# Kernel tuning notes

Measured on AMD Instinct MI355X. Metric: run time of the kernel, lower is better.

## Reference

```python
import jax, jax.numpy as jnp
import numpy as np

B, N, D = 64, 5000, 128
EPS = 1e-5

def setup_inputs() -> dict:
    key = jax.random.key(0)
    ks = jax.random.split(key, 10)
    s = 1.0 / np.sqrt(D)
    s2 = 1.0 / np.sqrt(2 * D)
    return {
        "batch_size": B,
        "num_customers": N,
        "solution_neighbours": jax.random.randint(ks[0], (B, N, 2), 0, N + 1),
        "embeddings": jax.random.normal(ks[1], (B, N + 1, D), dtype=jnp.float32),
        "w_left": jax.random.uniform(ks[2], (D, D), jnp.float32, -s, s),
        "w_right": jax.random.uniform(ks[3], (D, D), jnp.float32, -s, s),
        "w_comb": jax.random.uniform(ks[4], (D, 2 * D), jnp.float32, -s2, s2),
        "b_comb": jax.random.uniform(ks[5], (D,), jnp.float32, -s2, s2),
        "w_ff": jax.random.uniform(ks[6], (D, D), jnp.float32, -s, s),
        "b_ff": jax.random.uniform(ks[7], (D,), jnp.float32, -s, s),
        "norm_w": jnp.ones((D,), jnp.float32),
        "norm_b": jnp.zeros((D,), jnp.float32),
    }

def _gather(emb, idx):
    # emb: (B, N+1, D), idx: (B, N) -> (B, N, D)
    d = emb.shape[-1]
    return jnp.take_along_axis(emb, jnp.broadcast_to(idx[:, :, None], idx.shape + (d,)), axis=1)

def reference(batch_size, num_customers, solution_neighbours, embeddings,
              w_left, w_right, w_comb, b_comb, w_ff, b_ff, norm_w, norm_b):
    left = _gather(embeddings, solution_neighbours[:, :, 0])
    right = _gather(embeddings, solution_neighbours[:, :, 1])
    # per-edge linear projections (directed graph: separate weights)
    info = left @ w_left.T + right @ w_right.T        # (B, N, D)
    cust = embeddings[:, 1:]                           # (B, N, D)
    combined = jnp.concatenate([cust, info], axis=2)   # (B, N, 2D)
    h = jax.nn.relu(combined @ w_comb.T + b_comb)
    h = h @ w_ff.T + b_ff
    # residual + InstanceNorm1d over the customer axis (per batch, per channel)
    added = cust + h
    mean = jnp.mean(added, axis=1, keepdims=True)
    var = jnp.mean(jnp.square(added - mean), axis=1, keepdims=True)  # biased var
    normed = (added - mean) * jax.lax.rsqrt(var + EPS) * norm_w + norm_b
    return jnp.concatenate([embeddings[:, :1], normed], axis=1)
```

## Files before the change

### kernel.cpp

```cpp
#include <hip/hip_runtime.h>

typedef unsigned short u16;
typedef __attribute__((ext_vector_type(8))) short bf16x8;
typedef __attribute__((ext_vector_type(4))) float f32x4;

#define BB 64
#define NN 5000
#define DD 128
#define EROW 640128
#define CROW 640000

__device__ __forceinline__ u16 f2bf(float f){
  unsigned u = __builtin_bit_cast(unsigned, f);
  u += 0x7fffu + ((u >> 16) & 1u);
  return (u16)(u >> 16);
}
__device__ __forceinline__ float bf2f(u16 h){
  unsigned u = ((unsigned)h) << 16;
  return __builtin_bit_cast(float, u);
}

__global__ __launch_bounds__(256) void k0_prep(
    const float* __restrict__ wl, const float* __restrict__ wr,
    const float* __restrict__ wcmb, const float* __restrict__ wff,
    const float* __restrict__ emb, float* __restrict__ out,
    u16* __restrict__ wbf, float* __restrict__ sums, float* __restrict__ sumsq)
{
  int t = blockIdx.x * 256 + threadIdx.x;
  if      (t < 16384) wbf[t] = f2bf(wl[t]);
  else if (t < 32768) wbf[t] = f2bf(wr[t - 16384]);
  else if (t < 65536) wbf[t] = f2bf(wcmb[t - 32768]);
  else                wbf[t] = f2bf(wff[t - 65536]);
  if (t < 8192){
    sums[t] = 0.f; sumsq[t] = 0.f;
    int b = t >> 7, d = t & 127;
    out[(size_t)b * EROW + d] = emb[(size_t)b * EROW + d];
  }
}

template<bool BF>
__global__ __launch_bounds__(256, 4)
void k1_main(const int2* __restrict__ sol, const float* __restrict__ emb,
             const u16* __restrict__ wbf, const float* __restrict__ b_comb,
             const float* __restrict__ b_ff, float* __restrict__ out,
             u16* __restrict__ abuf, float* __restrict__ sums, float* __restrict__ sumsq)
{
  const int tid  = threadIdx.x;
  const int lane = tid & 63;
  const int wave = tid >> 6;
  const int q    = lane >> 4;
  const int c    = lane & 15;
  const int tile = blockIdx.x;
  const int b    = blockIdx.y;
  const int rbase = tile * 64;
  const int RC = min(64, NN - rbase);

  __shared__ u16 A[64][136];
  __shared__ u16 Bb[64][136];
  __shared__ int sIL[64], sIR[64];

  if (tid < 64){
    int r = rbase + tid; r = min(r, NN - 1);
    int2 p = sol[(size_t)b * NN + r];
    sIL[tid] = p.x; sIR[tid] = p.y;
  }
  __syncthreads();

  const float* embB = emb + (size_t)b * EROW;
  const int gi = tid >> 2, gsub = tid & 3;

  {
    int il = sIL[gi], ir = sIR[gi];
    const float4* vL = (const float4*)(embB + (size_t)il * DD) + gsub * 8;
    const float4* vR = (const float4*)(embB + (size_t)ir * DD) + gsub * 8;
    #pragma unroll
    for (int j = 0; j < 8; ++j){
      float4 a = vL[j], bb = vR[j];
      int col = gsub * 32 + j * 4;
      ushort4 ua = {f2bf(a.x),  f2bf(a.y),  f2bf(a.z),  f2bf(a.w)};
      ushort4 ub = {f2bf(bb.x), f2bf(bb.y), f2bf(bb.z), f2bf(bb.w)};
      *(ushort4*)&A[gi][col]  = ua;
      *(ushort4*)&Bb[gi][col] = ub;
    }
  }
  __syncthreads();

  const int n0 = wave * 32 + c;
  const int n1 = n0 + 16;

  const u16* wl = wbf;
  const u16* wr = wbf + 16384;
  const u16* wc = wbf + 32768;
  const u16* wf = wbf + 65536;

  const f32x4 fz = {0.f, 0.f, 0.f, 0.f};
  f32x4 acc[4][2];

  #pragma unroll
  for (int mt = 0; mt < 4; ++mt){ acc[mt][0] = fz; acc[mt][1] = fz; }
  #pragma unroll
  for (int ks = 0; ks < 8; ++ks){
    const u16* W = (ks < 4) ? wl : wr;
    const int kk = (ks & 3) * 32 + q * 8;
    bf16x8 b0 = *(const bf16x8*)(W + n0 * 128 + kk);
    bf16x8 b1 = *(const bf16x8*)(W + n1 * 128 + kk);
    #pragma unroll
    for (int mt = 0; mt < 4; ++mt){
      bf16x8 a = *(const bf16x8*)&((ks < 4) ? A : Bb)[mt * 16 + c][kk];
      acc[mt][0] = __builtin_amdgcn_mfma_f32_16x16x32_bf16(a, b0, acc[mt][0], 0, 0, 0);
      acc[mt][1] = __builtin_amdgcn_mfma_f32_16x16x32_bf16(a, b1, acc[mt][1], 0, 0, 0);
    }
  }
  __syncthreads();

  #pragma unroll
  for (int mt = 0; mt < 4; ++mt){
    #pragma unroll
    for (int r = 0; r < 4; ++r){
      int m = mt * 16 + q * 4 + r;
      A[m][n0] = f2bf(acc[mt][0][r]);
      A[m][n1] = f2bf(acc[mt][1][r]);
    }
  }
  {
    int crow = min(rbase + gi + 1, NN);
    const float4* vC = (const float4*)(embB + (size_t)crow * DD) + gsub * 8;
    #pragma unroll
    for (int j = 0; j < 8; ++j){
      float4 cc = vC[j];
      int col = gsub * 32 + j * 4;
      ushort4 uc = {f2bf(cc.x), f2bf(cc.y), f2bf(cc.z), f2bf(cc.w)};
      *(ushort4*)&Bb[gi][col] = uc;
    }
  }
  __syncthreads();

  #pragma unroll
  for (int mt = 0; mt < 4; ++mt){ acc[mt][0] = fz; acc[mt][1] = fz; }
  #pragma unroll
  for (int ks = 0; ks < 8; ++ks){
    const int kk = (ks & 3) * 32 + q * 8;
    const int kg = ks * 32 + q * 8;
    bf16x8 b0 = *(const bf16x8*)(wc + n0 * 256 + kg);
    bf16x8 b1 = *(const bf16x8*)(wc + n1 * 256 + kg);
    #pragma unroll
    for (int mt = 0; mt < 4; ++mt){
      bf16x8 a = *(const bf16x8*)&((ks < 4) ? Bb : A)[mt * 16 + c][kk];
      acc[mt][0] = __builtin_amdgcn_mfma_f32_16x16x32_bf16(a, b0, acc[mt][0], 0, 0, 0);
      acc[mt][1] = __builtin_amdgcn_mfma_f32_16x16x32_bf16(a, b1, acc[mt][1], 0, 0, 0);
    }
  }
  __syncthreads();
  {
    float bc0 = b_comb[n0], bc1 = b_comb[n1];
    #pragma unroll
    for (int mt = 0; mt < 4; ++mt){
      #pragma unroll
      for (int r = 0; r < 4; ++r){
        int m = mt * 16 + q * 4 + r;
        A[m][n0] = f2bf(fmaxf(acc[mt][0][r] + bc0, 0.f));
        A[m][n1] = f2bf(fmaxf(acc[mt][1][r] + bc1, 0.f));
      }
    }
  }
  __syncthreads();

  #pragma unroll
  for (int mt = 0; mt < 4; ++mt){ acc[mt][0] = fz; acc[mt][1] = fz; }
  #pragma unroll
  for (int ks = 0; ks < 4; ++ks){
    const int kk = ks * 32 + q * 8;
    bf16x8 b0 = *(const bf16x8*)(wf + n0 * 128 + kk);
    bf16x8 b1 = *(const bf16x8*)(wf + n1 * 128 + kk);
    #pragma unroll
    for (int mt = 0; mt < 4; ++mt){
      bf16x8 a = *(const bf16x8*)&A[mt * 16 + c][kk];
      acc[mt][0] = __builtin_amdgcn_mfma_f32_16x16x32_bf16(a, b0, acc[mt][0], 0, 0, 0);
      acc[mt][1] = __builtin_amdgcn_mfma_f32_16x16x32_bf16(a, b1, acc[mt][1], 0, 0, 0);
    }
  }

  const float bf0 = b_ff[n0], bf1 = b_ff[n1];
  float sv0 = 0.f, sq0 = 0.f, sv1 = 0.f, sq1 = 0.f;
  float* outB = out + (size_t)b * EROW;
  #pragma unroll
  for (int mt = 0; mt < 4; ++mt){
    #pragma unroll
    for (int r = 0; r < 4; ++r){
      int m = mt * 16 + q * 4 + r;
      float v0 = acc[mt][0][r] + bf0 + bf2f(Bb[m][n0]);
      float v1 = acc[mt][1][r] + bf1 + bf2f(Bb[m][n1]);
      acc[mt][0][r] = v0; acc[mt][1][r] = v1;
      if (m < RC){
        sv0 += v0; sq0 += v0 * v0;
        sv1 += v1; sq1 += v1 * v1;
        if (!BF){
          size_t ro = (size_t)(rbase + m + 1) * DD;
          outB[ro + n0] = v0;
          outB[ro + n1] = v1;
        }
      }
    }
  }
  sv0 += __shfl_xor(sv0, 16); sv0 += __shfl_xor(sv0, 32);
  sq0 += __shfl_xor(sq0, 16); sq0 += __shfl_xor(sq0, 32);
  sv1 += __shfl_xor(sv1, 16); sv1 += __shfl_xor(sv1, 32);
  sq1 += __shfl_xor(sq1, 16); sq1 += __shfl_xor(sq1, 32);
  if (q == 0){
    atomicAdd(&sums [b * DD + n0], sv0);
    atomicAdd(&sumsq[b * DD + n0], sq0);
    atomicAdd(&sums [b * DD + n1], sv1);
    atomicAdd(&sumsq[b * DD + n1], sq1);
  }

  if (BF){
    __syncthreads();
    #pragma unroll
    for (int mt = 0; mt < 4; ++mt){
      #pragma unroll
      for (int r = 0; r < 4; ++r){
        int m = mt * 16 + q * 4 + r;
        A[m][n0] = f2bf(acc[mt][0][r]);
        A[m][n1] = f2bf(acc[mt][1][r]);
      }
    }
    __syncthreads();
    const int row = tid >> 2, cb = tid & 3;
    if (rbase + row < NN){
      u16* dst = abuf + ((size_t)b * NN + rbase + row) * DD + cb * 32;
      #pragma unroll
      for (int j = 0; j < 4; ++j)
        *(bf16x8*)(dst + j * 8) = *(const bf16x8*)&A[row][cb * 32 + j * 8];
    }
  }
}

__global__ __launch_bounds__(256) void k1b_stats(
    const float* __restrict__ sums, const float* __restrict__ sumsq,
    const float* __restrict__ nw, const float* __restrict__ nb,
    float* __restrict__ scale, float* __restrict__ shift)
{
  int t = blockIdx.x * 256 + threadIdx.x;
  int d = t & 127;
  float mean = sums[t] * (1.f / NN);
  float var  = sumsq[t] * (1.f / NN) - mean * mean;
  float inv  = rsqrtf(var + 1e-5f);
  float sc = inv * nw[d];
  scale[t] = sc;
  shift[t] = nb[d] - mean * sc;
}

__global__ __launch_bounds__(256) void k2_bf(
    const u16* __restrict__ abuf, const float* __restrict__ scale,
    const float* __restrict__ shift, float* __restrict__ out)
{
  const int b = blockIdx.y;
  const int e = (blockIdx.x * 256 + threadIdx.x) * 8;
  if (e >= CROW) return;
  const int d = e & 127;
  const uint4 raw = *(const uint4*)(abuf + (size_t)b * CROW + e);
  const float4 s0 = *(const float4*)&scale[b * DD + d];
  const float4 s1 = *(const float4*)&scale[b * DD + d + 4];
  const float4 h0 = *(const float4*)&shift[b * DD + d];
  const float4 h1 = *(const float4*)&shift[b * DD + d + 4];
  float4 v0, v1;
  v0.x = __builtin_bit_cast(float, raw.x << 16);
  v0.y = __builtin_bit_cast(float, raw.x & 0xffff0000u);
  v0.z = __builtin_bit_cast(float, raw.y << 16);
  v0.w = __builtin_bit_cast(float, raw.y & 0xffff0000u);
  v1.x = __builtin_bit_cast(float, raw.z << 16);
  v1.y = __builtin_bit_cast(float, raw.z & 0xffff0000u);
  v1.z = __builtin_bit_cast(float, raw.w << 16);
  v1.w = __builtin_bit_cast(float, raw.w & 0xffff0000u);
  v0.x = v0.x * s0.x + h0.x; v0.y = v0.y * s0.y + h0.y;
  v0.z = v0.z * s0.z + h0.z; v0.w = v0.w * s0.w + h0.w;
  v1.x = v1.x * s1.x + h1.x; v1.y = v1.y * s1.y + h1.y;
  v1.z = v1.z * s1.z + h1.z; v1.w = v1.w * s1.w + h1.w;
  float4* p = (float4*)(out + (size_t)b * EROW + DD + e);
  p[0] = v0; p[1] = v1;
}

__global__ __launch_bounds__(256) void k2_rmw(
    float* __restrict__ out, const float* __restrict__ scale, const float* __restrict__ shift)
{
  const int b = blockIdx.y;
  const int e = (blockIdx.x * 256 + threadIdx.x) * 8;
  if (e >= CROW) return;
  const int d = e & 127;
  const float4 s0 = *(const float4*)&scale[b * DD + d];
  const float4 s1 = *(const float4*)&scale[b * DD + d + 4];
  const float4 h0 = *(const float4*)&shift[b * DD + d];
  const float4 h1 = *(const float4*)&shift[b * DD + d + 4];
  float4* p = (float4*)(out + (size_t)b * EROW + DD + e);
  float4 v0 = p[0], v1 = p[1];
  v0.x = v0.x * s0.x + h0.x; v0.y = v0.y * s0.y + h0.y;
  v0.z = v0.z * s0.z + h0.z; v0.w = v0.w * s0.w + h0.w;
  v1.x = v1.x * s1.x + h1.x; v1.y = v1.y * s1.y + h1.y;
  v1.z = v1.z * s1.z + h1.z; v1.w = v1.w * s1.w + h1.w;
  p[0] = v0; p[1] = v1;
}

extern "C" void kernel_launch(void* const* d_in, const int* in_sizes, int n_in,
                              void* d_out, int out_size, void* d_ws, size_t ws_size,
                              hipStream_t stream)
{
  const int2*  sol  = (const int2*) d_in[2];
  const float* emb  = (const float*)d_in[3];
  const float* wl   = (const float*)d_in[4];
  const float* wr   = (const float*)d_in[5];
  const float* wcmb = (const float*)d_in[6];
  const float* bcmb = (const float*)d_in[7];
  const float* wff  = (const float*)d_in[8];
  const float* bff  = (const float*)d_in[9];
  const float* nw   = (const float*)d_in[10];
  const float* nb   = (const float*)d_in[11];
  float* out = (float*)d_out;

  u16*   wbf   = (u16*)d_ws;
  float* sums  = (float*)((char*)d_ws + 163840);
  float* sumsq = (float*)((char*)d_ws + 196608);
  float* scale = (float*)((char*)d_ws + 229376);
  float* shift = (float*)((char*)d_ws + 262144);
  u16*   abuf  = (u16*)((char*)d_ws + 294912);

  const size_t need = 294912ull + (size_t)BB * NN * DD * 2;
  const bool bfpath = (ws_size >= need);

  k0_prep <<<320, 256, 0, stream>>>(wl, wr, wcmb, wff, emb, out, wbf, sums, sumsq);
  if (bfpath){
    k1_main<true> <<<dim3(79, 64), 256, 0, stream>>>(sol, emb, wbf, bcmb, bff, out, abuf, sums, sumsq);
    k1b_stats<<<32, 256, 0, stream>>>(sums, sumsq, nw, nb, scale, shift);
    k2_bf  <<<dim3(313, 64), 256, 0, stream>>>(abuf, scale, shift, out);
  } else {
    k1_main<false><<<dim3(79, 64), 256, 0, stream>>>(sol, emb, wbf, bcmb, bff, out, abuf, sums, sumsq);
    k1b_stats<<<32, 256, 0, stream>>>(sums, sumsq, nw, nb, scale, shift);
    k2_rmw <<<dim3(313, 64), 256, 0, stream>>>(out, scale, shift);
  }
}
```

Measured before the change: 482.2 us.

## Prefetch gathers and weights into registers ahead of each MFMA stage

Issues all three embedding row loads (left, right, customer) up front and packs them to bf16 in registers. Weight fragments for the next GEMM stage are loaded into register arrays before the current stage's barrier, so global-load latency overlaps compute and LDS writes. Launch bounds occupancy drops from 4 to 3 blocks per SM to make room for the extra registers. The risk is lower occupancy and register pressure hiding less latency overall.

```diff
diff --git a/kernel.cpp b/kernel.cpp
--- a/kernel.cpp
+++ b/kernel.cpp
@@ -18,6 +18,14 @@
 __device__ __forceinline__ float bf2f(u16 h){
   unsigned u = ((unsigned)h) << 16;
   return __builtin_bit_cast(float, u);
+}
+__device__ __forceinline__ bf16x8 pack8(float4 a, float4 b){
+  bf16x8 r;
+  r[0] = (short)f2bf(a.x); r[1] = (short)f2bf(a.y);
+  r[2] = (short)f2bf(a.z); r[3] = (short)f2bf(a.w);
+  r[4] = (short)f2bf(b.x); r[5] = (short)f2bf(b.y);
+  r[6] = (short)f2bf(b.z); r[7] = (short)f2bf(b.w);
+  return r;
 }
 
 __global__ __launch_bounds__(256) void k0_prep(
@@ -39,7 +47,7 @@
 }
 
 template<bool BF>
-__global__ __launch_bounds__(256, 4)
+__global__ __launch_bounds__(256, 3)
 void k1_main(const int2* __restrict__ sol, const float* __restrict__ emb,
              const u16* __restrict__ wbf, const float* __restrict__ b_comb,
              const float* __restrict__ b_ff, float* __restrict__ out,
@@ -69,47 +77,69 @@
   const float* embB = emb + (size_t)b * EROW;
   const int gi = tid >> 2, gsub = tid & 3;
 
+  const int n0 = wave * 32 + c;
+  const int n1 = n0 + 16;
+
+  const u16* wl = wbf;
+  const u16* wr = wbf + 16384;
+  const u16* wc = wbf + 32768;
+  const u16* wf = wbf + 65536;
+
+  const float bc0 = b_comb[n0], bc1 = b_comb[n1];
+  const float bf0 = b_ff[n0],  bf1 = b_ff[n1];
+
+  float4 la[8], ra[8], ca[8];
   {
     int il = sIL[gi], ir = sIR[gi];
     const float4* vL = (const float4*)(embB + (size_t)il * DD) + gsub * 8;
     const float4* vR = (const float4*)(embB + (size_t)ir * DD) + gsub * 8;
-    #pragma unroll
-    for (int j = 0; j < 8; ++j){
-      float4 a = vL[j], bb = vR[j];
-      int col = gsub * 32 + j * 4;
-      ushort4 ua = {f2bf(a.x),  f2bf(a.y),  f2bf(a.z),  f2bf(a.w)};
-      ushort4 ub = {f2bf(bb.x), f2bf(bb.y), f2bf(bb.z), f2bf(bb.w)};
-      *(ushort4*)&A[gi][col]  = ua;
-      *(ushort4*)&Bb[gi][col] = ub;
-    }
-  }
-  __syncthreads();
-
-  const int n0 = wave * 32 + c;
-  const int n1 = n0 + 16;
-
-  const u16* wl = wbf;
-  const u16* wr = wbf + 16384;
-  const u16* wc = wbf + 32768;
-  const u16* wf = wbf + 65536;
+    int crow = min(rbase + gi + 1, NN);
+    const float4* vC = (const float4*)(embB + (size_t)crow * DD) + gsub * 8;
+    #pragma unroll
+    for (int j = 0; j < 8; ++j) la[j] = vL[j];
+    #pragma unroll
+    for (int j = 0; j < 8; ++j) ra[j] = vR[j];
+    #pragma unroll
+    for (int j = 0; j < 8; ++j) ca[j] = vC[j];
+  }
+  #pragma unroll
+  for (int j = 0; j < 4; ++j){
+    *(bf16x8*)&A [gi][gsub * 32 + j * 8] = pack8(la[2*j], la[2*j+1]);
+    *(bf16x8*)&Bb[gi][gsub * 32 + j * 8] = pack8(ra[2*j], ra[2*j+1]);
+  }
+  bf16x8 cw[4];
+  #pragma unroll
+  for (int j = 0; j < 4; ++j) cw[j] = pack8(ca[2*j], ca[2*j+1]);
+  __syncthreads();
 
   const f32x4 fz = {0.f, 0.f, 0.f, 0.f};
   f32x4 acc[4][2];
-
-  #pragma unroll
-  for (int mt = 0; mt < 4; ++mt){ acc[mt][0] = fz; acc[mt][1] = fz; }
+  bf16x8 w0[8], w1[8];
+
   #pragma unroll
   for (int ks = 0; ks < 8; ++ks){
     const u16* W = (ks < 4) ? wl : wr;
     const int kk = (ks & 3) * 32 + q * 8;
-    bf16x8 b0 = *(const bf16x8*)(W + n0 * 128 + kk);
-    bf16x8 b1 = *(const bf16x8*)(W + n1 * 128 + kk);
+    w0[ks] = *(const bf16x8*)(W + n0 * 128 + kk);
+    w1[ks] = *(const bf16x8*)(W + n1 * 128 + kk);
+  }
+  #pragma unroll
+  for (int mt = 0; mt < 4; ++mt){ acc[mt][0] = fz; acc[mt][1] = fz; }
+  #pragma unroll
+  for (int ks = 0; ks < 8; ++ks){
+    const int kk = (ks & 3) * 32 + q * 8;
     #pragma unroll
     for (int mt = 0; mt < 4; ++mt){
       bf16x8 a = *(const bf16x8*)&((ks < 4) ? A : Bb)[mt * 16 + c][kk];
-      acc[mt][0] = __builtin_amdgcn_mfma_f32_16x16x32_bf16(a, b0, acc[mt][0], 0, 0, 0);
-      acc[mt][1] = __builtin_amdgcn_mfma_f32_16x16x32_bf16(a, b1, acc[mt][1], 0, 0, 0);
-    }
+      acc[mt][0] = __builtin_amdgcn_mfma_f32_16x16x32_bf16(a, w0[ks], acc[mt][0], 0, 0, 0);
+      acc[mt][1] = __builtin_amdgcn_mfma_f32_16x16x32_bf16(a, w1[ks], acc[mt][1], 0, 0, 0);
+    }
+  }
+  #pragma unroll
+  for (int ks = 0; ks < 8; ++ks){
+    const int kg = ks * 32 + q * 8;
+    w0[ks] = *(const bf16x8*)(wc + n0 * 256 + kg);
+    w1[ks] = *(const bf16x8*)(wc + n1 * 256 + kg);
   }
   __syncthreads();
 
@@ -122,17 +152,9 @@
       A[m][n1] = f2bf(acc[mt][1][r]);
     }
   }
-  {
-    int crow = min(rbase + gi + 1, NN);
-    const float4* vC = (const float4*)(embB + (size_t)crow * DD) + gsub * 8;
-    #pragma unroll
-    for (int j = 0; j < 8; ++j){
-      float4 cc = vC[j];
-      int col = gsub * 32 + j * 4;
-      ushort4 uc = {f2bf(cc.x), f2bf(cc.y), f2bf(cc.z), f2bf(cc.w)};
-      *(ushort4*)&Bb[gi][col] = uc;
-    }
-  }
+  #pragma unroll
+  for (int j = 0; j < 4; ++j)
+    *(bf16x8*)&Bb[gi][gsub * 32 + j * 8] = cw[j];
   __syncthreads();
 
   #pragma unroll
@@ -140,47 +162,44 @@
   #pragma unroll
   for (int ks = 0; ks < 8; ++ks){
     const int kk = (ks & 3) * 32 + q * 8;
-    const int kg = ks * 32 + q * 8;
-    bf16x8 b0 = *(const bf16x8*)(wc + n0 * 256 + kg);
-    bf16x8 b1 = *(const bf16x8*)(wc + n1 * 256 + kg);
     #pragma unroll
     for (int mt = 0; mt < 4; ++mt){
       bf16x8 a = *(const bf16x8*)&((ks < 4) ? Bb : A)[mt * 16 + c][kk];
-      acc[mt][0] = __builtin_amdgcn_mfma_f32_16x16x32_bf16(a, b0, acc[mt][0], 0, 0, 0);
-      acc[mt][1] = __builtin_amdgcn_mfma_f32_16x16x32_bf16(a, b1, acc[mt][1], 0, 0, 0);
-    }
-  }
-  __syncthreads();
-  {
-    float bc0 = b_comb[n0], bc1 = b_comb[n1];
-    #pragma unroll
-    for (int mt = 0; mt < 4; ++mt){
-      #pragma unroll
-      for (int r = 0; r < 4; ++r){
-        int m = mt * 16 + q * 4 + r;
-        A[m][n0] = f2bf(fmaxf(acc[mt][0][r] + bc0, 0.f));
-        A[m][n1] = f2bf(fmaxf(acc[mt][1][r] + bc1, 0.f));
-      }
-    }
-  }
-  __syncthreads();
-
-  #pragma unroll
-  for (int mt = 0; mt < 4; ++mt){ acc[mt][0] = fz; acc[mt][1] = fz; }
+      acc[mt][0] = __builtin_amdgcn_mfma_f32_16x16x32_bf16(a, w0[ks], acc[mt][0], 0, 0, 0);
+      acc[mt][1] = __builtin_amdgcn_mfma_f32_16x16x32_bf16(a, w1[ks], acc[mt][1], 0, 0, 0);
+    }
+  }
   #pragma unroll
   for (int ks = 0; ks < 4; ++ks){
     const int kk = ks * 32 + q * 8;
-    bf16x8 b0 = *(const bf16x8*)(wf + n0 * 128 + kk);
-    bf16x8 b1 = *(const bf16x8*)(wf + n1 * 128 + kk);
+    w0[ks] = *(const bf16x8*)(wf + n0 * 128 + kk);
+    w1[ks] = *(const bf16x8*)(wf + n1 * 128 + kk);
+  }
+  __syncthreads();
+  #pragma unroll
+  for (int mt = 0; mt < 4; ++mt){
+    #pragma unroll
+    for (int r = 0; r < 4; ++r){
+      int m = mt * 16 + q * 4 + r;
+      A[m][n0] = f2bf(fmaxf(acc[mt][0][r] + bc0, 0.f));
+      A[m][n1] = f2bf(fmaxf(acc[mt][1][r] + bc1, 0.f));
+    }
+  }
+  __syncthreads();
+
+  #pragma unroll
+  for (int mt = 0; mt < 4; ++mt){ acc[mt][0] = fz; acc[mt][1] = fz; }
+  #pragma unroll
+  for (int ks = 0; ks < 4; ++ks){
+    const int kk = ks * 32 + q * 8;
     #pragma unroll
     for (int mt = 0; mt < 4; ++mt){
       bf16x8 a = *(const bf16x8*)&A[mt * 16 + c][kk];
-      acc[mt][0] = __builtin_amdgcn_mfma_f32_16x16x32_bf16(a, b0, acc[mt][0], 0, 0, 0);
-      acc[mt][1] = __builtin_amdgcn_mfma_f32_16x16x32_bf16(a, b1, acc[mt][1], 0, 0, 0);
-    }
-  }
-
-  const float bf0 = b_ff[n0], bf1 = b_ff[n1];
+      acc[mt][0] = __builtin_amdgcn_mfma_f32_16x16x32_bf16(a, w0[ks], acc[mt][0], 0, 0, 0);
+      acc[mt][1] = __builtin_amdgcn_mfma_f32_16x16x32_bf16(a, w1[ks], acc[mt][1], 0, 0, 0);
+    }
+  }
+
   float sv0 = 0.f, sq0 = 0.f, sv1 = 0.f, sq1 = 0.f;
   float* outB = out + (size_t)b * EROW;
   #pragma unroll
```

New measurement: 473.9 us. No clear change (-1.7%).

## Process two tiles per block with register prefetch of next gathers; fuse stats into normalize

Applied to the files above, without the earlier changes.

The main kernel now launches half as many blocks, and each block handles two 64-row tiles. The neighbour gathers for the second tile are prefetched into registers while the first tile's last GEMM and epilogue run, which is meant to hide gather latency. Custom barriers replace __syncthreads. The separate stats kernel is removed: each normalize block recomputes scale and shift into shared memory, saving one launch at the cost of redundant small work. Launch bounds drop to 3 blocks/SM to fit the extra prefetch registers, which reduces occupancy.

```diff
diff --git a/kernel.cpp b/kernel.cpp
--- a/kernel.cpp
+++ b/kernel.cpp
@@ -9,6 +9,12 @@
 #define DD 128
 #define EROW 640128
 #define CROW 640000
+#define NT 79
+#define HT 40
+
+#define BAR() do{ asm volatile("s_waitcnt lgkmcnt(0)" ::: "memory"); \
+                  __builtin_amdgcn_s_barrier();                      \
+                  __builtin_amdgcn_sched_barrier(0); }while(0)
 
 __device__ __forceinline__ u16 f2bf(float f){
   unsigned u = __builtin_bit_cast(unsigned, f);
@@ -18,6 +24,14 @@
 __device__ __forceinline__ float bf2f(u16 h){
   unsigned u = ((unsigned)h) << 16;
   return __builtin_bit_cast(float, u);
+}
+__device__ __forceinline__ bf16x8 pack8(float4 a, float4 b){
+  bf16x8 r;
+  r[0] = (short)f2bf(a.x); r[1] = (short)f2bf(a.y);
+  r[2] = (short)f2bf(a.z); r[3] = (short)f2bf(a.w);
+  r[4] = (short)f2bf(b.x); r[5] = (short)f2bf(b.y);
+  r[6] = (short)f2bf(b.z); r[7] = (short)f2bf(b.w);
+  return r;
 }
 
 __global__ __launch_bounds__(256) void k0_prep(
@@ -39,7 +53,7 @@
 }
 
 template<bool BF>
-__global__ __launch_bounds__(256, 4)
+__global__ __launch_bounds__(256, 3)
 void k1_main(const int2* __restrict__ sol, const float* __restrict__ emb,
              const u16* __restrict__ wbf, const float* __restrict__ b_comb,
              const float* __restrict__ b_ff, float* __restrict__ out,
@@ -50,40 +64,13 @@
   const int wave = tid >> 6;
   const int q    = lane >> 4;
   const int c    = lane & 15;
-  const int tile = blockIdx.x;
   const int b    = blockIdx.y;
-  const int rbase = tile * 64;
-  const int RC = min(64, NN - rbase);
 
   __shared__ u16 A[64][136];
   __shared__ u16 Bb[64][136];
-  __shared__ int sIL[64], sIR[64];
-
-  if (tid < 64){
-    int r = rbase + tid; r = min(r, NN - 1);
-    int2 p = sol[(size_t)b * NN + r];
-    sIL[tid] = p.x; sIR[tid] = p.y;
-  }
-  __syncthreads();
 
   const float* embB = emb + (size_t)b * EROW;
   const int gi = tid >> 2, gsub = tid & 3;
-
-  {
-    int il = sIL[gi], ir = sIR[gi];
-    const float4* vL = (const float4*)(embB + (size_t)il * DD) + gsub * 8;
-    const float4* vR = (const float4*)(embB + (size_t)ir * DD) + gsub * 8;
-    #pragma unroll
-    for (int j = 0; j < 8; ++j){
-      float4 a = vL[j], bb = vR[j];
-      int col = gsub * 32 + j * 4;
-      ushort4 ua = {f2bf(a.x),  f2bf(a.y),  f2bf(a.z),  f2bf(a.w)};
-      ushort4 ub = {f2bf(bb.x), f2bf(bb.y), f2bf(bb.z), f2bf(bb.w)};
-      *(ushort4*)&A[gi][col]  = ua;
-      *(ushort4*)&Bb[gi][col] = ub;
-    }
-  }
-  __syncthreads();
 
   const int n0 = wave * 32 + c;
   const int n1 = n0 + 16;
@@ -93,66 +80,101 @@
   const u16* wc = wbf + 32768;
   const u16* wf = wbf + 65536;
 
+  const float bc0 = b_comb[n0], bc1 = b_comb[n1];
+  const float bf0 = b_ff[n0],  bf1 = b_ff[n1];
+
+  int tile = blockIdx.x;
+
+  float4 pl[8], pr[8];
+  {
+    int r0 = min(tile * 64 + gi, NN - 1);
+    int2 p = sol[(size_t)b * NN + r0];
+    const float4* vL = (const float4*)(embB + (size_t)p.x * DD) + gsub * 8;
+    const float4* vR = (const float4*)(embB + (size_t)p.y * DD) + gsub * 8;
+    #pragma unroll
+    for (int j = 0; j < 8; ++j) pl[j] = vL[j];
+    #pragma unroll
+    for (int j = 0; j < 8; ++j) pr[j] = vR[j];
+  }
+
   const f32x4 fz = {0.f, 0.f, 0.f, 0.f};
-  f32x4 acc[4][2];
 
   #pragma unroll
-  for (int mt = 0; mt < 4; ++mt){ acc[mt][0] = fz; acc[mt][1] = fz; }
-  #pragma unroll
-  for (int ks = 0; ks < 8; ++ks){
-    const u16* W = (ks < 4) ? wl : wr;
-    const int kk = (ks & 3) * 32 + q * 8;
-    bf16x8 b0 = *(const bf16x8*)(W + n0 * 128 + kk);
-    bf16x8 b1 = *(const bf16x8*)(W + n1 * 128 + kk);
+  for (int it = 0; it < 2; ++it){
+    const int rbase = tile * 64;
+    const int RC = min(64, NN - rbase);
+
+    if (it) BAR();
+
+    float4 ca[8];
+    {
+      int crow = min(rbase + gi + 1, NN);
+      const float4* vC = (const float4*)(embB + (size_t)crow * DD) + gsub * 8;
+      #pragma unroll
+      for (int j = 0; j < 8; ++j) ca[j] = vC[j];
+    }
+    int2 pnx = {0, 0};
+    if (it == 0 && tile + HT < NT){
+      int r0 = min((tile + HT) * 64 + gi, NN - 1);
+      pnx = sol[(size_t)b * NN + r0];
+    }
+
+    #pragma unroll
+    for (int j = 0; j < 4; ++j){
+      *(bf16x8*)&A [gi][gsub * 32 + j * 8] = pack8(pl[2*j], pl[2*j+1]);
+      *(bf16x8*)&Bb[gi][gsub * 32 + j * 8] = pack8(pr[2*j], pr[2*j+1]);
+    }
+    BAR();
+
+    f32x4 acc[4][2];
+
+    #pragma unroll
+    for (int mt = 0; mt < 4; ++mt){ acc[mt][0] = fz; acc[mt][1] = fz; }
+    #pragma unroll
+    for (int ks = 0; ks < 8; ++ks){
+      const u16* W = (ks < 4) ? wl : wr;
+      const int kk = (ks & 3) * 32 + q * 8;
+      bf16x8 b0 = *(const bf16x8*)(W + n0 * 128 + kk);
+      bf16x8 b1 = *(const bf16x8*)(W + n1 * 128 + kk);
+      #pragma unroll
+      for (int mt = 0; mt < 4; ++mt){
+        bf16x8 a = *(const bf16x8*)&((ks < 4) ? A : Bb)[mt * 16 + c][kk];
+        acc[mt][0] = __builtin_amdgcn_mfma_f32_16x16x32_bf16(a, b0, acc[mt][0], 0, 0, 0);
+        acc[mt][1] = __builtin_amdgcn_mfma_f32_16x16x32_bf16(a, b1, acc[mt][1], 0, 0, 0);
+      }
+    }
+    BAR();
+
     #pragma unroll
     for (int mt = 0; mt < 4; ++mt){
-      bf16x8 a = *(const bf16x8*)&((ks < 4) ? A : Bb)[mt * 16 + c][kk];
-      acc[mt][0] = __builtin_amdgcn_mfma_f32_16x16x32_bf16(a, b0, acc[mt][0], 0, 0, 0);
-      acc[mt][1] = __builtin_amdgcn_mfma_f32_16x16x32_bf16(a, b1, acc[mt][1], 0, 0, 0);
-    }
-  }
-  __syncthreads();
-
-  #pragma unroll
-  for (int mt = 0; mt < 4; ++mt){
-    #pragma unroll
-    for (int r = 0; r < 4; ++r){
-      int m = mt * 16 + q * 4 + r;
-      A[m][n0] = f2bf(acc[mt][0][r]);
-      A[m][n1] = f2bf(acc[mt][1][r]);
-    }
-  }
-  {
-    int crow = min(rbase + gi + 1, NN);
-    const float4* vC = (const float4*)(embB + (size_t)crow * DD) + gsub * 8;
-    #pragma unroll
-    for (int j = 0; j < 8; ++j){
-      float4 cc = vC[j];
-      int col = gsub * 32 + j * 4;
-      ushort4 uc = {f2bf(cc.x), f2bf(cc.y), f2bf(cc.z), f2bf(cc.w)};
-      *(ushort4*)&Bb[gi][col] = uc;
-    }
-  }
-  __syncthreads();
-
-  #pragma unroll
-  for (int mt = 0; mt < 4; ++mt){ acc[mt][0] = fz; acc[mt][1] = fz; }
-  #pragma unroll
-  for (int ks = 0; ks < 8; ++ks){
-    const int kk = (ks & 3) * 32 + q * 8;
-    const int kg = ks * 32 + q * 8;
-    bf16x8 b0 = *(const bf16x8*)(wc + n0 * 256 + kg);
-    bf16x8 b1 = *(const bf16x8*)(wc + n1 * 256 + kg);
-    #pragma unroll
-    for (int mt = 0; mt < 4; ++mt){
-      bf16x8 a = *(const bf16x8*)&((ks < 4) ? Bb : A)[mt * 16 + c][kk];
-      acc[mt][0] = __builtin_amdgcn_mfma_f32_16x16x32_bf16(a, b0, acc[mt][0], 0, 0, 0);
-      acc[mt][1] = __builtin_amdgcn_mfma_f32_16x16x32_bf16(a, b1, acc[mt][1], 0, 0, 0);
-    }
-  }
-  __syncthreads();
-  {
-    float bc0 = b_comb[n0], bc1 = b_comb[n1];
+      #pragma unroll
+      for (int r = 0; r < 4; ++r){
+        int m = mt * 16 + q * 4 + r;
+        A[m][n0] = f2bf(acc[mt][0][r]);
+        A[m][n1] = f2bf(acc[mt][1][r]);
+      }
+    }
+    #pragma unroll
+    for (int j = 0; j < 4; ++j)
+      *(bf16x8*)&Bb[gi][gsub * 32 + j * 8] = pack8(ca[2*j], ca[2*j+1]);
+    BAR();
+
+    #pragma unroll
+    for (int mt = 0; mt < 4; ++mt){ acc[mt][0] = fz; acc[mt][1] = fz; }
+    #pragma unroll
+    for (int ks = 0; ks < 8; ++ks){
+      const int kk = (ks & 3) * 32 + q * 8;
+      const int kg = ks * 32 + q * 8;
+      bf16x8 b0 = *(const bf16x8*)(wc + n0 * 256 + kg);
+      bf16x8 b1 = *(const bf16x8*)(wc + n1 * 256 + kg);
+      #pragma unroll
+      for (int mt = 0; mt < 4; ++mt){
+        bf16x8 a = *(const bf16x8*)&((ks < 4) ? Bb : A)[mt * 16 + c][kk];
+        acc[mt][0] = __builtin_amdgcn_mfma_f32_16x16x32_bf16(a, b0, acc[mt][0], 0, 0, 0);
+        acc[mt][1] = __builtin_amdgcn_mfma_f32_16x16x32_bf16(a, b1, acc[mt][1], 0, 0, 0);
+      }
+    }
+    BAR();
     #pragma unroll
     for (int mt = 0; mt < 4; ++mt){
       #pragma unroll
@@ -162,107 +184,117 @@
         A[m][n1] = f2bf(fmaxf(acc[mt][1][r] + bc1, 0.f));
       }
     }
-  }
-  __syncthreads();
-
-  #pragma unroll
-  for (int mt = 0; mt < 4; ++mt){ acc[mt][0] = fz; acc[mt][1] = fz; }
-  #pragma unroll
-  for (int ks = 0; ks < 4; ++ks){
-    const int kk = ks * 32 + q * 8;
-    bf16x8 b0 = *(const bf16x8*)(wf + n0 * 128 + kk);
-    bf16x8 b1 = *(const bf16x8*)(wf + n1 * 128 + kk);
-    #pragma unroll
-    for (int mt = 0; mt < 4; ++mt){
-      bf16x8 a = *(const bf16x8*)&A[mt * 16 + c][kk];
-      acc[mt][0] = __builtin_amdgcn_mfma_f32_16x16x32_bf16(a, b0, acc[mt][0], 0, 0, 0);
-      acc[mt][1] = __builtin_amdgcn_mfma_f32_16x16x32_bf16(a, b1, acc[mt][1], 0, 0, 0);
-    }
-  }
-
-  const float bf0 = b_ff[n0], bf1 = b_ff[n1];
-  float sv0 = 0.f, sq0 = 0.f, sv1 = 0.f, sq1 = 0.f;
-  float* outB = out + (size_t)b * EROW;
-  #pragma unroll
-  for (int mt = 0; mt < 4; ++mt){
-    #pragma unroll
-    for (int r = 0; r < 4; ++r){
-      int m = mt * 16 + q * 4 + r;
-      float v0 = acc[mt][0][r] + bf0 + bf2f(Bb[m][n0]);
-      float v1 = acc[mt][1][r] + bf1 + bf2f(Bb[m][n1]);
-      acc[mt][0][r] = v0; acc[mt][1][r] = v1;
-      if (m < RC){
-        sv0 += v0; sq0 += v0 * v0;
-        sv1 += v1; sq1 += v1 * v1;
-        if (!BF){
-          size_t ro = (size_t)(rbase + m + 1) * DD;
-          outB[ro + n0] = v0;
-          outB[ro + n1] = v1;
-        }
-      }
-    }
-  }
-  sv0 += __shfl_xor(sv0, 16); sv0 += __shfl_xor(sv0, 32);
-  sq0 += __shfl_xor(sq0, 16); sq0 += __shfl_xor(sq0, 32);
-  sv1 += __shfl_xor(sv1, 16); sv1 += __shfl_xor(sv1, 32);
-  sq1 += __shfl_xor(sq1, 16); sq1 += __shfl_xor(sq1, 32);
-  if (q == 0){
-    atomicAdd(&sums [b * DD + n0], sv0);
-    atomicAdd(&sumsq[b * DD + n0], sq0);
-    atomicAdd(&sums [b * DD + n1], sv1);
-    atomicAdd(&sumsq[b * DD + n1], sq1);
-  }
-
-  if (BF){
-    __syncthreads();
+    BAR();
+
+    #pragma unroll
+    for (int mt = 0; mt < 4; ++mt){ acc[mt][0] = fz; acc[mt][1] = fz; }
+    #pragma unroll
+    for (int ks = 0; ks < 4; ++ks){
+      const int kk = ks * 32 + q * 8;
+      bf16x8 b0 = *(const bf16x8*)(wf + n0 * 128 + kk);
+      bf16x8 b1 = *(const bf16x8*)(wf + n1 * 128 + kk);
+      #pragma unroll
+      for (int mt = 0; mt < 4; ++mt){
+        bf16x8 a = *(const bf16x8*)&A[mt * 16 + c][kk];
+        acc[mt][0] = __builtin_amdgcn_mfma_f32_16x16x32_bf16(a, b0, acc[mt][0], 0, 0, 0);
+        acc[mt][1] = __builtin_amdgcn_mfma_f32_16x16x32_bf16(a, b1, acc[mt][1], 0, 0, 0);
+      }
+    }
+
+    __builtin_amdgcn_sched_barrier(0);
+    if (it == 0 && tile + HT < NT){
+      const float4* vL = (const float4*)(embB + (size_t)pnx.x * DD) + gsub * 8;
+      const float4* vR = (const float4*)(embB + (size_t)pnx.y * DD) + gsub * 8;
+      #pragma unroll
+      for (int j = 0; j < 8; ++j) pl[j] = vL[j];
+      #pragma unroll
+      for (int j = 0; j < 8; ++j) pr[j] = vR[j];
+    }
+    __builtin_amdgcn_sched_barrier(0);
+
+    float sv0 = 0.f, sq0 = 0.f, sv1 = 0.f, sq1 = 0.f;
+    float* outB = out + (size_t)b * EROW;
     #pragma unroll
     for (int mt = 0; mt < 4; ++mt){
       #pragma unroll
       for (int r = 0; r < 4; ++r){
         int m = mt * 16 + q * 4 + r;
-        A[m][n0] = f2bf(acc[mt][0][r]);
-        A[m][n1] = f2bf(acc[mt][1][r]);
-      }
-    }
-    __syncthreads();
-    const int row = tid >> 2, cb = tid & 3;
-    if (rbase + row < NN){
-      u16* dst = abuf + ((size_t)b * NN + rbase + row) * DD + cb * 32;
-      #pragma unroll
-      for (int j = 0; j < 4; ++j)
-        *(bf16x8*)(dst + j * 8) = *(const bf16x8*)&A[row][cb * 32 + j * 8];
-    }
-  }
-}
-
-__global__ __launch_bounds__(256) void k1b_stats(
-    const float* __restrict__ sums, const float* __restrict__ sumsq,
-    const float* __restrict__ nw, const float* __restrict__ nb,
-    float* __restrict__ scale, float* __restrict__ shift)
-{
-  int t = blockIdx.x * 256 + threadIdx.x;
-  int d = t & 127;
-  float mean = sums[t] * (1.f / NN);
-  float var  = sumsq[t] * (1.f / NN) - mean * mean;
-  float inv  = rsqrtf(var + 1e-5f);
-  float sc = inv * nw[d];
-  scale[t] = sc;
-  shift[t] = nb[d] - mean * sc;
+        float v0 = acc[mt][0][r] + bf0 + bf2f(Bb[m][n0]);
+        float v1 = acc[mt][1][r] + bf1 + bf2f(Bb[m][n1]);
+        acc[mt][0][r] = v0; acc[mt][1][r] = v1;
+        if (m < RC){
+          sv0 += v0; sq0 += v0 * v0;
+          sv1 += v1; sq1 += v1 * v1;
+          if (!BF){
+            size_t ro = (size_t)(rbase + m + 1) * DD;
+            outB[ro + n0] = v0;
+            outB[ro + n1] = v1;
+          }
+        }
+      }
+    }
+    sv0 += __shfl_xor(sv0, 16); sv0 += __shfl_xor(sv0, 32);
+    sq0 += __shfl_xor(sq0, 16); sq0 += __shfl_xor(sq0, 32);
+    sv1 += __shfl_xor(sv1, 16); sv1 += __shfl_xor(sv1, 32);
+    sq1 += __shfl_xor(sq1, 16); sq1 += __shfl_xor(sq1, 32);
+    if (q == 0){
+      atomicAdd(&sums [b * DD + n0], sv0);
+      atomicAdd(&sumsq[b * DD + n0], sq0);
+      atomicAdd(&sums [b * DD + n1], sv1);
+      atomicAdd(&sumsq[b * DD + n1], sq1);
+    }
+
+    if (BF){
+      BAR();
+      #pragma unroll
+      for (int mt = 0; mt < 4; ++mt){
+        #pragma unroll
+        for (int r = 0; r < 4; ++r){
+          int m = mt * 16 + q * 4 + r;
+          A[m][n0] = f2bf(acc[mt][0][r]);
+          A[m][n1] = f2bf(acc[mt][1][r]);
+        }
+      }
+      BAR();
+      const int row = tid >> 2, cb = tid & 3;
+      if (rbase + row < NN){
+        u16* dst = abuf + ((size_t)b * NN + rbase + row) * DD + cb * 32;
+        #pragma unroll
+        for (int j = 0; j < 4; ++j)
+          *(bf16x8*)(dst + j * 8) = *(const bf16x8*)&A[row][cb * 32 + j * 8];
+      }
+    }
+
+    tile += HT;
+    if (tile >= NT) break;
+  }
 }
 
 __global__ __launch_bounds__(256) void k2_bf(
-    const u16* __restrict__ abuf, const float* __restrict__ scale,
-    const float* __restrict__ shift, float* __restrict__ out)
-{
+    const u16* __restrict__ abuf, const float* __restrict__ sums,
+    const float* __restrict__ sumsq, const float* __restrict__ nw,
+    const float* __restrict__ nb, float* __restrict__ out)
+{
+  __shared__ float ssc[128], ssh[128];
   const int b = blockIdx.y;
-  const int e = (blockIdx.x * 256 + threadIdx.x) * 8;
+  const int t = threadIdx.x;
+  if (t < 128){
+    float mean = sums[b * DD + t] * (1.f / NN);
+    float var  = sumsq[b * DD + t] * (1.f / NN) - mean * mean;
+    float inv  = rsqrtf(var + 1e-5f);
+    float sc   = inv * nw[t];
+    ssc[t] = sc;
+    ssh[t] = nb[t] - mean * sc;
+  }
+  __syncthreads();
+  const int e = (blockIdx.x * 256 + t) * 8;
   if (e >= CROW) return;
   const int d = e & 127;
   const uint4 raw = *(const uint4*)(abuf + (size_t)b * CROW + e);
-  const float4 s0 = *(const float4*)&scale[b * DD + d];
-  const float4 s1 = *(const float4*)&scale[b * DD + d + 4];
-  const float4 h0 = *(const float4*)&shift[b * DD + d];
-  const float4 h1 = *(const float4*)&shift[b * DD + d + 4];
+  const float4 s0 = *(const float4*)&ssc[d];
+  const float4 s1 = *(const float4*)&ssc[d + 4];
+  const float4 h0 = *(const float4*)&ssh[d];
+  const float4 h1 = *(const float4*)&ssh[d + 4];
   float4 v0, v1;
   v0.x = __builtin_bit_cast(float, raw.x << 16);
   v0.y = __builtin_bit_cast(float, raw.x & 0xffff0000u);
@@ -281,16 +313,29 @@
 }
 
 __global__ __launch_bounds__(256) void k2_rmw(
-    float* __restrict__ out, const float* __restrict__ scale, const float* __restrict__ shift)
-{
+    float* __restrict__ out, const float* __restrict__ sums,
+    const float* __restrict__ sumsq, const float* __restrict__ nw,
+    const float* __restrict__ nb)
+{
+  __shared__ float ssc[128], ssh[128];
   const int b = blockIdx.y;
-  const int e = (blockIdx.x * 256 + threadIdx.x) * 8;
+  const int t = threadIdx.x;
+  if (t < 128){
+    float mean = sums[b * DD + t] * (1.f / NN);
+    float var  = sumsq[b * DD + t] * (1.f / NN) - mean * mean;
+    float inv  = rsqrtf(var + 1e-5f);
+    float sc   = inv * nw[t];
+    ssc[t] = sc;
+    ssh[t] = nb[t] - mean * sc;
+  }
+  __syncthreads();
+  const int e = (blockIdx.x * 256 + t) * 8;
   if (e >= CROW) return;
   const int d = e & 127;
-  const float4 s0 = *(const float4*)&scale[b * DD + d];
-  const float4 s1 = *(const float4*)&scale[b * DD + d + 4];
-  const float4 h0 = *(const float4*)&shift[b * DD + d];
-  const float4 h1 = *(const float4*)&shift[b * DD + d + 4];
+  const float4 s0 = *(const float4*)&ssc[d];
+  const float4 s1 = *(const float4*)&ssc[d + 4];
+  const float4 h0 = *(const float4*)&ssh[d];
+  const float4 h1 = *(const float4*)&ssh[d + 4];
   float4* p = (float4*)(out + (size_t)b * EROW + DD + e);
   float4 v0 = p[0], v1 = p[1];
   v0.x = v0.x * s0.x + h0.x; v0.y = v0.y * s0.y + h0.y;
@@ -319,8 +364,6 @@
   u16*   wbf   = (u16*)d_ws;
   float* sums  = (float*)((char*)d_ws + 163840);
   float* sumsq = (float*)((char*)d_ws + 196608);
-  float* scale = (float*)((char*)d_ws + 229376);
-  float* shift = (float*)((char*)d_ws + 262144);
   u16*   abuf  = (u16*)((char*)d_ws + 294912);
 
   const size_t need = 294912ull + (size_t)BB * NN * DD * 2;
@@ -328,12 +371,10 @@
 
   k0_prep <<<320, 256, 0, stream>>>(wl, wr, wcmb, wff, emb, out, wbf, sums, sumsq);
   if (bfpath){
-    k1_main<true> <<<dim3(79, 64), 256, 0, stream>>>(sol, emb, wbf, bcmb, bff, out, abuf, sums, sumsq);
-    k1b_stats<<<32, 256, 0, stream>>>(sums, sumsq, nw, nb, scale, shift);
-    k2_bf  <<<dim3(313, 64), 256, 0, stream>>>(abuf, scale, shift, out);
+    k1_main<true> <<<dim3(HT, BB), 256, 0, stream>>>(sol, emb, wbf, bcmb, bff, out, abuf, sums, sumsq);
+    k2_bf  <<<dim3(313, 64), 256, 0, stream>>>(abuf, sums, sumsq, nw, nb, out);
   } else {
-    k1_main<false><<<dim3(79, 64), 256, 0, stream>>>(sol, emb, wbf, bcmb, bff, out, abuf, sums, sumsq);
-    k1b_stats<<<32, 256, 0, stream>>>(sums, sumsq, nw, nb, scale, shift);
-    k2_rmw <<<dim3(313, 64), 256, 0, stream>>>(out, scale, shift);
-  }
-}
+    k1_main<false><<<dim3(HT, BB), 256, 0, stream>>>(sol, emb, wbf, bcmb, bff, out, abuf, sums, sumsq);
+    k2_rmw <<<dim3(313, 64), 256, 0, stream>>>(out, sums, sumsq, nw, nb);
+  }
+}
```

New measurement: 478.5 us. Within noise of the previous version (-0.8%).
